# Kernel optimization log

Measured on AMD Instinct MI355X. Metric: run time of the kernel, lower is better.

## Reference

```python
import jax, jax.numpy as jnp
import numpy as np

B, S, D, E, H = 2, 1024, 1024, 16, 2048  # batch, seq, in_dim, num_experts, hidden_dim
TOP_K = 2
TEMP = 1.0


def setup_inputs() -> dict:
    key = jax.random.key(0)
    ks = jax.random.split(key, 4)
    sc_d = 1.0 / np.sqrt(D)
    sc_h = 1.0 / np.sqrt(H)
    return {
        "x": jax.random.normal(ks[0], (B, S, D), dtype=jnp.float32),
        "Wr": jax.random.normal(ks[1], (D, E), dtype=jnp.float32) * sc_d,  # router
        "br": jnp.zeros((E,), dtype=jnp.float32),
        "W1": jax.random.normal(ks[2], (E, D, H), dtype=jnp.float32) * sc_d,  # expert fc1
        "b1": jnp.zeros((E, H), dtype=jnp.float32),
        "W2": jax.random.normal(ks[3], (E, H, D), dtype=jnp.float32) * sc_h,  # expert fc2
        "b2": jnp.zeros((E, D), dtype=jnp.float32),
    }


def reference(x, Wr, br, W1, b1, W2, b2):
    token_shape = x.shape[:-1]
    d = x.shape[-1]
    xt = x.reshape(-1, d)  # [T, D] flattened tokens
    T = xt.shape[0]

    # Router: logits / temperature -> softmax -> top-k
    logits = (xt @ Wr + br) / TEMP
    probs = jax.nn.softmax(logits, axis=-1)          # [T, E]
    w, idx = jax.lax.top_k(probs, TOP_K)             # [T, K]
    w = w / jnp.clip(jnp.sum(w, axis=-1, keepdims=True), 1e-9)

    # Combine weights per (token, expert); top-k indices are unique per row
    comb = jnp.zeros((T, E), dtype=xt.dtype)
    comb = comb.at[jnp.arange(T)[:, None], idx].add(w)  # [T, E]

    # Per-expert 2-layer MLP with exact (erf) GELU, matching torch nn.GELU
    h = jax.nn.gelu(jnp.einsum('td,edh->teh', xt, W1) + b1, approximate=False)  # [T, E, H]
    o = jnp.einsum('teh,eho->teo', h, W2) + b2                                   # [T, E, D]
    y = jnp.einsum('teo,te->to', o, comb)                                        # [T, D]

    # residual (in_dim == out_dim)
    y = xt + y
    return y.reshape(*token_shape, d)
```

## Files before the change

### kernel.cpp

```cpp
#include <hip/hip_runtime.h>
#include <hip/hip_bf16.h>

#define T_TOK 2048
#define DIM   1024
#define NEXP  16
#define HID   2048
#define MAXMT 32

typedef __attribute__((ext_vector_type(8))) short short8;
typedef __attribute__((ext_vector_type(4))) float f32x4;

__device__ __forceinline__ unsigned short f2bf(float f) {
  __hip_bfloat16 h = __float2bfloat16(f);
  union { __hip_bfloat16 b; unsigned short u; } cv; cv.b = h; return cv.u;
}

__device__ __forceinline__ void glds16(const void* g, void* l) {
  __builtin_amdgcn_global_load_lds(
      (const __attribute__((address_space(1))) unsigned int*)g,
      (__attribute__((address_space(3))) unsigned int*)l, 16, 0, 0);
}

__global__ __launch_bounds__(256) void router_k(const float* __restrict__ x,
    const float* __restrict__ Wr, const float* __restrict__ br,
    int* __restrict__ re, float* __restrict__ rwv, int* __restrict__ cnt)
{
  __shared__ float wl[NEXP][DIM + 1];
  const int tid = threadIdx.x;
#pragma unroll
  for (int i = 0; i < 16; i++) {
    const int flat = tid + 256 * i;
    const int d = flat >> 2, e4 = (flat & 3) * 4;
    float4 v = *reinterpret_cast<const float4*>(Wr + (size_t)d * NEXP + e4);
    wl[e4 + 0][d] = v.x; wl[e4 + 1][d] = v.y;
    wl[e4 + 2][d] = v.z; wl[e4 + 3][d] = v.w;
  }
  __syncthreads();
  const int wid = tid >> 6, lane = tid & 63;
  for (int tt = 0; tt < 8; tt++) {
    const int t = blockIdx.x * 32 + wid * 8 + tt;
    const float* xr = x + (size_t)t * DIM;
    float acc[NEXP];
#pragma unroll
    for (int e = 0; e < NEXP; e++) acc[e] = 0.f;
    for (int i = 0; i < DIM / 64; i++) {
      const int d = lane + 64 * i;
      const float xv = xr[d];
#pragma unroll
      for (int e = 0; e < NEXP; e++) acc[e] += xv * wl[e][d];
    }
#pragma unroll
    for (int e = 0; e < NEXP; e++) {
      float v = acc[e];
      v += __shfl_xor(v, 32); v += __shfl_xor(v, 16); v += __shfl_xor(v, 8);
      v += __shfl_xor(v, 4);  v += __shfl_xor(v, 2);  v += __shfl_xor(v, 1);
      acc[e] = v;
    }
    if (lane == 0) {
      float lg[NEXP];
#pragma unroll
      for (int e = 0; e < NEXP; e++) lg[e] = acc[e] + br[e];
      int e0 = 0; float b0 = lg[0];
      for (int e = 1; e < NEXP; e++) if (lg[e] > b0) { b0 = lg[e]; e0 = e; }
      int e1 = (e0 == 0) ? 1 : 0; float b1v = lg[e1];
      for (int e = 0; e < NEXP; e++) if (e != e0 && lg[e] > b1v) { b1v = lg[e]; e1 = e; }
      float p1 = expf(b1v - b0);
      float inv = 1.0f / (1.0f + p1);
      re[2*t] = e0; re[2*t+1] = e1;
      rwv[2*t] = inv; rwv[2*t+1] = p1 * inv;
      atomicAdd(&cnt[e0], 1); atomicAdd(&cnt[e1], 1);
    }
  }
}

__global__ void scan_k(const int* cnt, int* basev, int* tile_e, int* tile_m0, int* ntt) {
  if (threadIdx.x == 0) {
    int s = 0, t = 0;
    for (int e = 0; e < NEXP; e++) {
      basev[e] = s;
      for (int m0 = 0; m0 < cnt[e]; m0 += 256) { tile_e[t] = e; tile_m0[t] = m0; t++; }
      s += cnt[e];
    }
    ntt[0] = t;
  }
}

__global__ __launch_bounds__(256) void scatter_k(const int* __restrict__ re,
    const float* __restrict__ rwv, const int* __restrict__ basev, int* fill,
    int* __restrict__ rows_token, float* __restrict__ rows_w, int* __restrict__ slot_of)
{
  int t = blockIdx.x * 256 + threadIdx.x;
  if (t >= T_TOK) return;
  for (int k = 0; k < 2; k++) {
    int e = re[2*t+k];
    int pos = atomicAdd(&fill[e], 1);
    int row = basev[e] + pos;
    rows_token[row] = t;
    rows_w[row] = rwv[2*t+k];
    slot_of[2*t+k] = row;
  }
}

__global__ __launch_bounds__(256) void conv_k(const float* __restrict__ x,
                                              unsigned short* __restrict__ xg)
{
  const int row = blockIdx.x, t = threadIdx.x;
  float4 v = reinterpret_cast<const float4*>(x + (size_t)row * DIM)[t];
  ushort4 h;
  h.x = f2bf(v.x); h.y = f2bf(v.y); h.z = f2bf(v.z); h.w = f2bf(v.w);
  reinterpret_cast<ushort4*>(xg + (size_t)row * DIM)[t] = h;
}

template<bool FC1>
__global__ __launch_bounds__(256, 2) void expert_gemm_k(
    const unsigned short* __restrict__ Ag,
    const float* __restrict__ Wg,
    const float* __restrict__ bg,
    const int* __restrict__ cnt, const int* __restrict__ basev,
    const int* __restrict__ tile_e, const int* __restrict__ tile_m0,
    const int* __restrict__ ntt, const float* __restrict__ rows_w,
    const int* __restrict__ rows_token,
    unsigned short* __restrict__ hout, float* __restrict__ obuf)
{
  constexpr int KD = FC1 ? DIM : HID;
  constexpr int ND = FC1 ? HID : DIM;
  constexpr int KSPL = FC1 ? 1 : 2;
  constexpr int KLOC = KD / KSPL;
  constexpr int BM = 256, BN = 64, BK = 64, LDPB = 68;
  constexpr int NPH = KLOC / BK;
  if ((int)blockIdx.y >= ntt[0]) return;
  const int e  = tile_e[blockIdx.y], m0 = tile_m0[blockIdx.y];
  const int Ne = cnt[e], base = basev[e];
  const int nt = blockIdx.x, kz = blockIdx.z;
  const int kbase = kz * KLOC;
  __shared__ unsigned short As[BM][BK];
  __shared__ unsigned short Bs[BN][LDPB];
  const int tid = threadIdx.x, lane = tid & 63, wid = tid >> 6;

  const int lrow = lane >> 3;
  const int lchunk = ((lane & 7) ^ (lrow & 7)) * 8;
  const unsigned short* asrc[8];
  unsigned short* aldst[8];
#pragma unroll
  for (int j = 0; j < 8; j++) {
    const int r = j * 32 + wid * 8 + lrow;
    int g = m0 + r; if (g >= Ne) g = Ne - 1;
    if constexpr (FC1) {
      const int tok = rows_token[base + g];
      asrc[j] = Ag + (size_t)tok * KD + kbase + lchunk;
    } else {
      asrc[j] = Ag + (size_t)(base + g) * KD + kbase + lchunk;
    }
    aldst[j] = &As[j * 32 + wid * 8][0];
  }
  const int bn4 = (tid & 15) * 4, bkr = tid >> 4;
  const float* bsrc = Wg + (size_t)e * KD * ND + (size_t)(kbase + bkr) * ND
                      + nt * BN + bn4;

  const int lr = lane & 15, lg = lane >> 4;
  const bool wactive = (m0 + wid * 64) < Ne;

  const unsigned short* afp[4][2];
#pragma unroll
  for (int m = 0; m < 4; m++)
#pragma unroll
    for (int h = 0; h < 2; h++)
      afp[m][h] = &As[wid * 64 + m * 16 + lr][(((lg + 4*h) ^ (lr & 7)) * 8)];

  f32x4 acc[4][4];
#pragma unroll
  for (int m = 0; m < 4; m++)
#pragma unroll
    for (int n = 0; n < 4; n++) acc[m][n] = (f32x4){0.f, 0.f, 0.f, 0.f};

  float4 bst[4];
#define LOADB(K0)                                                            \
  { _Pragma("unroll")                                                        \
    for (int j = 0; j < 4; j++)                                              \
      bst[j] = *reinterpret_cast<const float4*>(bsrc + (size_t)((K0) + 16 * j) * ND); }

  LOADB(0)

  for (int ph = 0; ph < NPH; ++ph) {
    const int k0 = ph * BK;
    __syncthreads();
#pragma unroll
    for (int j = 0; j < 8; j++) glds16(asrc[j] + k0, aldst[j]);
#pragma unroll
    for (int j = 0; j < 4; j++) {
      Bs[bn4 + 0][bkr + 16 * j] = f2bf(bst[j].x);
      Bs[bn4 + 1][bkr + 16 * j] = f2bf(bst[j].y);
      Bs[bn4 + 2][bkr + 16 * j] = f2bf(bst[j].z);
      Bs[bn4 + 3][bkr + 16 * j] = f2bf(bst[j].w);
    }
    __syncthreads();
    if (ph + 1 < NPH) LOADB((ph + 1) * BK)
    if (wactive) {
      __builtin_amdgcn_s_setprio(1);
#pragma unroll
      for (int h = 0; h < 2; h++) {
        short8 af[4], bb[4];
#pragma unroll
        for (int m = 0; m < 4; m++)
          af[m] = *reinterpret_cast<const short8*>(afp[m][h]);
#pragma unroll
        for (int n = 0; n < 4; n++)
          bb[n] = *reinterpret_cast<const short8*>(&Bs[n * 16 + lr][(lg + 4*h) * 8]);
#pragma unroll
        for (int m = 0; m < 4; m++)
#pragma unroll
          for (int n = 0; n < 4; n++)
            acc[m][n] = __builtin_amdgcn_mfma_f32_16x16x32_bf16(af[m], bb[n],
                                                                acc[m][n], 0, 0, 0);
      }
      __builtin_amdgcn_s_setprio(0);
    }
  }
#undef LOADB

  if (!wactive) return;
#pragma unroll
  for (int n = 0; n < 4; n++) {
    const int col = nt * BN + n * 16 + lr;
    const float bias = (kz == 0) ? bg[(size_t)e * ND + col] : 0.f;
#pragma unroll
    for (int m = 0; m < 4; m++) {
      const int rbase = m0 + wid * 64 + m * 16 + lg * 4;
#pragma unroll
      for (int v = 0; v < 4; v++) {
        const int r = rbase + v;
        if (r < Ne) {
          float val = acc[m][n][v] + bias;
          if constexpr (FC1) {
            val = 0.5f * val * (1.0f + erff(val * 0.70710678118654752440f));
            hout[(size_t)(base + r) * HID + col] = f2bf(val);
          } else {
            obuf[(size_t)kz * (2 * T_TOK) * DIM + (size_t)(base + r) * DIM + col]
                = val * rows_w[base + r];
          }
        }
      }
    }
  }
}

__global__ __launch_bounds__(256) void combine_k(const float* __restrict__ x,
    const float* __restrict__ obuf, const int* __restrict__ slot_of,
    float* __restrict__ out)
{
  const int t = blockIdx.x, c = threadIdx.x;
  const int s0 = slot_of[2*t], s1 = slot_of[2*t+1];
  const size_t PSZ = (size_t)(2 * T_TOK) * DIM;
  const float4 a  = reinterpret_cast<const float4*>(x + (size_t)t * DIM)[c];
  const float4 p0 = reinterpret_cast<const float4*>(obuf + (size_t)s0 * DIM)[c];
  const float4 p1 = reinterpret_cast<const float4*>(obuf + PSZ + (size_t)s0 * DIM)[c];
  const float4 q0 = reinterpret_cast<const float4*>(obuf + (size_t)s1 * DIM)[c];
  const float4 q1 = reinterpret_cast<const float4*>(obuf + PSZ + (size_t)s1 * DIM)[c];
  float4 r;
  r.x = a.x + p0.x + p1.x + q0.x + q1.x;
  r.y = a.y + p0.y + p1.y + q0.y + q1.y;
  r.z = a.z + p0.z + p1.z + q0.z + q1.z;
  r.w = a.w + p0.w + p1.w + q0.w + q1.w;
  reinterpret_cast<float4*>(out + (size_t)t * DIM)[c] = r;
}

extern "C" void kernel_launch(void* const* d_in, const int* in_sizes, int n_in,
                              void* d_out, int out_size, void* d_ws, size_t ws_size,
                              hipStream_t stream) {
  const float* x  = (const float*)d_in[0];
  const float* Wr = (const float*)d_in[1];
  const float* br = (const float*)d_in[2];
  const float* W1 = (const float*)d_in[3];
  const float* b1 = (const float*)d_in[4];
  const float* W2 = (const float*)d_in[5];
  const float* b2 = (const float*)d_in[6];
  float* out = (float*)d_out;
  char* ws = (char*)d_ws;

  int*   cnt        = (int*)  (ws + 0);
  int*   fill       = (int*)  (ws + 64);
  int*   basev      = (int*)  (ws + 128);
  int*   ntt        = (int*)  (ws + 192);
  int*   tile_e     = (int*)  (ws + 1024);
  int*   tile_m0    = (int*)  (ws + 2048);
  int*   re         = (int*)  (ws + 16384);
  float* rwv        = (float*)(ws + 32768);
  int*   rows_token = (int*)  (ws + 49152);
  float* rows_w     = (float*)(ws + 65536);
  int*   slot_of    = (int*)  (ws + 81920);
  unsigned short* xg   = (unsigned short*)(ws + ((size_t)(1 << 17)));
  unsigned short* hbuf = (unsigned short*)(ws + ((size_t)(1 << 17) + ((size_t)8  << 20)));
  float*          obuf = (float*)         (ws + ((size_t)(1 << 17) + ((size_t)24 << 20)));

  hipMemsetAsync(ws, 0, 256, stream);
  router_k<<<dim3(T_TOK / 32), dim3(256), 0, stream>>>(x, Wr, br, re, rwv, cnt);
  scan_k<<<dim3(1), dim3(64), 0, stream>>>(cnt, basev, tile_e, tile_m0, ntt);
  scatter_k<<<dim3(T_TOK / 256), dim3(256), 0, stream>>>(re, rwv, basev, fill,
                                                         rows_token, rows_w, slot_of);
  conv_k<<<dim3(T_TOK), dim3(256), 0, stream>>>(x, xg);
  expert_gemm_k<true><<<dim3(HID / 64, MAXMT, 1), dim3(256), 0, stream>>>(
      xg, W1, b1, cnt, basev, tile_e, tile_m0, ntt, rows_w, rows_token, hbuf, obuf);
  expert_gemm_k<false><<<dim3(DIM / 64, MAXMT, 2), dim3(256), 0, stream>>>(
      hbuf, W2, b2, cnt, basev, tile_e, tile_m0, ntt, rows_w, rows_token, hbuf, obuf);
  combine_k<<<dim3(T_TOK), dim3(256), 0, stream>>>(x, obuf, slot_of, out);
}
```

Baseline: 223.7 us.

## Widen expert GEMM tiles to 512 threads, add split-K to FC1 with separate GELU pass

Each expert GEMM block now runs 8 waves on a 256x128 tile, so every fp32 weight tile converted to bf16 feeds twice as many output columns. FC1 now splits K in two and writes bf16 partials, and a new gelu_k kernel sums them and applies the exact GELU. FC2 splits K four ways and stores bf16 partials, which combine_k sums. The aim is to halve redundant weight loads and conversions per output and raise parallelism. The cost is an extra launch, more partial-buffer traffic, and bf16 rounding of the pre-activation and output partials, which adds error.

```diff
diff --git a/kernel.cpp b/kernel.cpp
--- a/kernel.cpp
+++ b/kernel.cpp
@@ -13,6 +13,9 @@
 __device__ __forceinline__ unsigned short f2bf(float f) {
   __hip_bfloat16 h = __float2bfloat16(f);
   union { __hip_bfloat16 b; unsigned short u; } cv; cv.b = h; return cv.u;
+}
+__device__ __forceinline__ float bf2f(unsigned short u) {
+  union { unsigned int i; float f; } cv; cv.i = ((unsigned int)u) << 16; return cv.f;
 }
 
 __device__ __forceinline__ void glds16(const void* g, void* l) {
@@ -112,7 +115,7 @@
 }
 
 template<bool FC1>
-__global__ __launch_bounds__(256, 2) void expert_gemm_k(
+__global__ __launch_bounds__(512, 2) void expert_gemm_k(
     const unsigned short* __restrict__ Ag,
     const float* __restrict__ Wg,
     const float* __restrict__ bg,
@@ -120,13 +123,13 @@
     const int* __restrict__ tile_e, const int* __restrict__ tile_m0,
     const int* __restrict__ ntt, const float* __restrict__ rows_w,
     const int* __restrict__ rows_token,
-    unsigned short* __restrict__ hout, float* __restrict__ obuf)
+    unsigned short* __restrict__ pout)
 {
   constexpr int KD = FC1 ? DIM : HID;
   constexpr int ND = FC1 ? HID : DIM;
-  constexpr int KSPL = FC1 ? 1 : 2;
+  constexpr int KSPL = FC1 ? 2 : 4;
   constexpr int KLOC = KD / KSPL;
-  constexpr int BM = 256, BN = 64, BK = 64, LDPB = 68;
+  constexpr int BM = 256, BN = 128, BK = 64, LDPB = 68;
   constexpr int NPH = KLOC / BK;
   if ((int)blockIdx.y >= ntt[0]) return;
   const int e  = tile_e[blockIdx.y], m0 = tile_m0[blockIdx.y];
@@ -139,11 +142,11 @@
 
   const int lrow = lane >> 3;
   const int lchunk = ((lane & 7) ^ (lrow & 7)) * 8;
-  const unsigned short* asrc[8];
-  unsigned short* aldst[8];
-#pragma unroll
-  for (int j = 0; j < 8; j++) {
-    const int r = j * 32 + wid * 8 + lrow;
+  const unsigned short* asrc[4];
+  unsigned short* aldst[4];
+#pragma unroll
+  for (int j = 0; j < 4; j++) {
+    const int r = wid * 32 + j * 8 + lrow;
     int g = m0 + r; if (g >= Ne) g = Ne - 1;
     if constexpr (FC1) {
       const int tok = rows_token[base + g];
@@ -151,21 +154,22 @@
     } else {
       asrc[j] = Ag + (size_t)(base + g) * KD + kbase + lchunk;
     }
-    aldst[j] = &As[j * 32 + wid * 8][0];
-  }
-  const int bn4 = (tid & 15) * 4, bkr = tid >> 4;
+    aldst[j] = &As[wid * 32 + j * 8][0];
+  }
+  const int bn4 = (tid & 31) * 4, bkr = tid >> 5;
   const float* bsrc = Wg + (size_t)e * KD * ND + (size_t)(kbase + bkr) * ND
                       + nt * BN + bn4;
 
+  const int wr = wid >> 1, wc = wid & 1;
   const int lr = lane & 15, lg = lane >> 4;
-  const bool wactive = (m0 + wid * 64) < Ne;
+  const bool wactive = (m0 + wr * 64) < Ne;
 
   const unsigned short* afp[4][2];
 #pragma unroll
   for (int m = 0; m < 4; m++)
 #pragma unroll
     for (int h = 0; h < 2; h++)
-      afp[m][h] = &As[wid * 64 + m * 16 + lr][(((lg + 4*h) ^ (lr & 7)) * 8)];
+      afp[m][h] = &As[wr * 64 + m * 16 + lr][(((lg + 4*h) ^ (lr & 7)) * 8)];
 
   f32x4 acc[4][4];
 #pragma unroll
@@ -185,7 +189,7 @@
     const int k0 = ph * BK;
     __syncthreads();
 #pragma unroll
-    for (int j = 0; j < 8; j++) glds16(asrc[j] + k0, aldst[j]);
+    for (int j = 0; j < 4; j++) glds16(asrc[j] + k0, aldst[j]);
 #pragma unroll
     for (int j = 0; j < 4; j++) {
       Bs[bn4 + 0][bkr + 16 * j] = f2bf(bst[j].x);
@@ -205,7 +209,8 @@
           af[m] = *reinterpret_cast<const short8*>(afp[m][h]);
 #pragma unroll
         for (int n = 0; n < 4; n++)
-          bb[n] = *reinterpret_cast<const short8*>(&Bs[n * 16 + lr][(lg + 4*h) * 8]);
+          bb[n] = *reinterpret_cast<const short8*>(
+              &Bs[wc * 64 + n * 16 + lr][(lg + 4*h) * 8]);
 #pragma unroll
         for (int m = 0; m < 4; m++)
 #pragma unroll
@@ -219,48 +224,68 @@
 #undef LOADB
 
   if (!wactive) return;
+  constexpr size_t PSZ = (size_t)(2 * T_TOK) * ND;
 #pragma unroll
   for (int n = 0; n < 4; n++) {
-    const int col = nt * BN + n * 16 + lr;
+    const int col = nt * BN + wc * 64 + n * 16 + lr;
     const float bias = (kz == 0) ? bg[(size_t)e * ND + col] : 0.f;
 #pragma unroll
     for (int m = 0; m < 4; m++) {
-      const int rbase = m0 + wid * 64 + m * 16 + lg * 4;
+      const int rbase = m0 + wr * 64 + m * 16 + lg * 4;
 #pragma unroll
       for (int v = 0; v < 4; v++) {
         const int r = rbase + v;
         if (r < Ne) {
           float val = acc[m][n][v] + bias;
-          if constexpr (FC1) {
-            val = 0.5f * val * (1.0f + erff(val * 0.70710678118654752440f));
-            hout[(size_t)(base + r) * HID + col] = f2bf(val);
-          } else {
-            obuf[(size_t)kz * (2 * T_TOK) * DIM + (size_t)(base + r) * DIM + col]
-                = val * rows_w[base + r];
-          }
+          if constexpr (!FC1) val *= rows_w[base + r];
+          pout[(size_t)kz * PSZ + (size_t)(base + r) * ND + col] = f2bf(val);
         }
       }
     }
   }
 }
 
+__global__ __launch_bounds__(256) void gelu_k(const unsigned short* __restrict__ hpart,
+                                              unsigned short* __restrict__ hbuf)
+{
+  const size_t PSZ = (size_t)(2 * T_TOK) * HID;
+  const size_t off = (size_t)blockIdx.x * HID + threadIdx.x * 8;
+  ushort4 a0 = *reinterpret_cast<const ushort4*>(hpart + off);
+  ushort4 a1 = *reinterpret_cast<const ushort4*>(hpart + off + 4);
+  ushort4 b0 = *reinterpret_cast<const ushort4*>(hpart + PSZ + off);
+  ushort4 b1 = *reinterpret_cast<const ushort4*>(hpart + PSZ + off + 4);
+  unsigned short o[8];
+  float v;
+#define G(UA, UB, I)                                                         \
+  v = bf2f(UA) + bf2f(UB);                                                   \
+  v = 0.5f * v * (1.0f + erff(v * 0.70710678118654752440f));                 \
+  o[I] = f2bf(v);
+  G(a0.x, b0.x, 0) G(a0.y, b0.y, 1) G(a0.z, b0.z, 2) G(a0.w, b0.w, 3)
+  G(a1.x, b1.x, 4) G(a1.y, b1.y, 5) G(a1.z, b1.z, 6) G(a1.w, b1.w, 7)
+#undef G
+  *reinterpret_cast<ushort4*>(hbuf + off)     = *reinterpret_cast<ushort4*>(&o[0]);
+  *reinterpret_cast<ushort4*>(hbuf + off + 4) = *reinterpret_cast<ushort4*>(&o[4]);
+}
+
 __global__ __launch_bounds__(256) void combine_k(const float* __restrict__ x,
-    const float* __restrict__ obuf, const int* __restrict__ slot_of,
+    const unsigned short* __restrict__ opart, const int* __restrict__ slot_of,
     float* __restrict__ out)
 {
   const int t = blockIdx.x, c = threadIdx.x;
   const int s0 = slot_of[2*t], s1 = slot_of[2*t+1];
   const size_t PSZ = (size_t)(2 * T_TOK) * DIM;
-  const float4 a  = reinterpret_cast<const float4*>(x + (size_t)t * DIM)[c];
-  const float4 p0 = reinterpret_cast<const float4*>(obuf + (size_t)s0 * DIM)[c];
-  const float4 p1 = reinterpret_cast<const float4*>(obuf + PSZ + (size_t)s0 * DIM)[c];
-  const float4 q0 = reinterpret_cast<const float4*>(obuf + (size_t)s1 * DIM)[c];
-  const float4 q1 = reinterpret_cast<const float4*>(obuf + PSZ + (size_t)s1 * DIM)[c];
-  float4 r;
-  r.x = a.x + p0.x + p1.x + q0.x + q1.x;
-  r.y = a.y + p0.y + p1.y + q0.y + q1.y;
-  r.z = a.z + p0.z + p1.z + q0.z + q1.z;
-  r.w = a.w + p0.w + p1.w + q0.w + q1.w;
+  const float4 a = reinterpret_cast<const float4*>(x + (size_t)t * DIM)[c];
+  float r0 = a.x, r1 = a.y, r2 = a.z, r3 = a.w;
+#pragma unroll
+  for (int kz = 0; kz < 4; kz++) {
+    ushort4 p = *reinterpret_cast<const ushort4*>(
+        opart + kz * PSZ + (size_t)s0 * DIM + c * 4);
+    r0 += bf2f(p.x); r1 += bf2f(p.y); r2 += bf2f(p.z); r3 += bf2f(p.w);
+    ushort4 q = *reinterpret_cast<const ushort4*>(
+        opart + kz * PSZ + (size_t)s1 * DIM + c * 4);
+    r0 += bf2f(q.x); r1 += bf2f(q.y); r2 += bf2f(q.z); r3 += bf2f(q.w);
+  }
+  float4 r; r.x = r0; r.y = r1; r.z = r2; r.w = r3;
   reinterpret_cast<float4*>(out + (size_t)t * DIM)[c] = r;
 }
 
@@ -288,9 +313,10 @@
   int*   rows_token = (int*)  (ws + 49152);
   float* rows_w     = (float*)(ws + 65536);
   int*   slot_of    = (int*)  (ws + 81920);
-  unsigned short* xg   = (unsigned short*)(ws + ((size_t)(1 << 17)));
-  unsigned short* hbuf = (unsigned short*)(ws + ((size_t)(1 << 17) + ((size_t)8  << 20)));
-  float*          obuf = (float*)         (ws + ((size_t)(1 << 17) + ((size_t)24 << 20)));
+  unsigned short* xg    = (unsigned short*)(ws + ((size_t)(1 << 17)));
+  unsigned short* hbuf  = (unsigned short*)(ws + ((size_t)(1 << 17) + ((size_t)8   << 20)));
+  unsigned short* hpart = (unsigned short*)(ws + ((size_t)(1 << 17) + ((size_t)24  << 20)));
+  unsigned short* opart = (unsigned short*)(ws + ((size_t)(1 << 17) + ((size_t)56  << 20)));
 
   hipMemsetAsync(ws, 0, 256, stream);
   router_k<<<dim3(T_TOK / 32), dim3(256), 0, stream>>>(x, Wr, br, re, rwv, cnt);
@@ -298,9 +324,10 @@
   scatter_k<<<dim3(T_TOK / 256), dim3(256), 0, stream>>>(re, rwv, basev, fill,
                                                          rows_token, rows_w, slot_of);
   conv_k<<<dim3(T_TOK), dim3(256), 0, stream>>>(x, xg);
-  expert_gemm_k<true><<<dim3(HID / 64, MAXMT, 1), dim3(256), 0, stream>>>(
-      xg, W1, b1, cnt, basev, tile_e, tile_m0, ntt, rows_w, rows_token, hbuf, obuf);
-  expert_gemm_k<false><<<dim3(DIM / 64, MAXMT, 2), dim3(256), 0, stream>>>(
-      hbuf, W2, b2, cnt, basev, tile_e, tile_m0, ntt, rows_w, rows_token, hbuf, obuf);
-  combine_k<<<dim3(T_TOK), dim3(256), 0, stream>>>(x, obuf, slot_of, out);
-}
+  expert_gemm_k<true><<<dim3(HID / 128, MAXMT, 2), dim3(512), 0, stream>>>(
+      xg, W1, b1, cnt, basev, tile_e, tile_m0, ntt, rows_w, rows_token, hpart);
+  gelu_k<<<dim3(2 * T_TOK), dim3(256), 0, stream>>>(hpart, hbuf);
+  expert_gemm_k<false><<<dim3(DIM / 128, MAXMT, 4), dim3(512), 0, stream>>>(
+      hbuf, W2, b2, cnt, basev, tile_e, tile_m0, ntt, rows_w, rows_token, opart);
+  combine_k<<<dim3(T_TOK), dim3(256), 0, stream>>>(x, opart, slot_of, out);
+}
```

Result: slower. 282.5 us (+26.3%).
